# Kernel optimization log

Measured on AMD Instinct MI355X. Metric: run time of the kernel, lower is better.

The kernel has to match this reference:

```python
import jax, jax.numpy as jnp
import numpy as np

N = 16384      # batch size
F = 1024       # n_features
H = 256        # n_dim (latent)


def setup_inputs() -> dict:
    key = jax.random.key(0)
    ks = jax.random.split(key, 6)
    X = jax.random.normal(ks[0], (N, F), dtype=jnp.float32)
    We = jax.random.normal(ks[1], (F, H), dtype=jnp.float32) / np.sqrt(F).astype(np.float32)
    be = jnp.zeros((H,), dtype=jnp.float32)
    Wd = jax.random.normal(ks[2], (H, F), dtype=jnp.float32) / np.sqrt(H).astype(np.float32)
    bd = jnp.zeros((F,), dtype=jnp.float32)
    Wc = jax.random.normal(ks[3], (H, 1), dtype=jnp.float32) / np.sqrt(H).astype(np.float32)
    bc = jnp.zeros((1,), dtype=jnp.float32)
    s = jax.random.randint(ks[4], (N,), 0, 2, dtype=jnp.int32)  # protected attribute labels in {0,1}
    return {"X": X, "We": We, "be": be, "Wd": Wd, "bd": bd, "Wc": Wc, "bc": bc, "s": s, "p": 1}


def reference(X, We, be, Wd, bd, Wc, bc, s, p):
    # encoder / decoder (single Linear each, as in the default NRL construction)
    g = X @ We + be                      # [N, H]
    rec = g @ Wd + bd                    # [N, F]
    mse_mean = jnp.mean((rec - X) ** 2)  # MSELoss is built with reduction='sum' but forward uses torch.mean(pow(...)) directly

    # critic scores for ALL rows (critics share weights: [module]*n_protected)
    c = (g @ Wc + bc)[:, 0]              # [N]

    # masked pairwise L1: sum_{i in P, j notin P} |c_i - c_j|
    mp = (s == p)                        # rows where s == p
    mpf = mp.astype(c.dtype)
    mrf = (~mp).astype(c.dtype)
    Dmat = jnp.abs(c[:, None] - c[None, :])   # [N, N] pairwise L1 (cdist equivalent)
    total = mpf @ (Dmat @ mrf)                # mp^T D mr == cdist(c_p, c_rest, p=1).sum()

    w_dist_count = mp.sum()                   # == w_dist.shape[0] (number of protected rows)
    w_dist_mean = total / w_dist_count.astype(c.dtype)

    return (mse_mean, jnp.asarray(rec.shape[0]), w_dist_mean, w_dist_count)
```

## Files before the change

### kernel.cpp

```cpp
#include <hip/hip_runtime.h>
#include <hip/hip_bf16.h>
#include <cstdint>

#define NR 16384
#define NF 1024
#define NH 256

typedef __bf16 bf16x8 __attribute__((ext_vector_type(8)));
typedef float f32x4 __attribute__((ext_vector_type(4)));
typedef unsigned short us8 __attribute__((ext_vector_type(8)));

static __device__ __forceinline__ unsigned short f2bf(float f) {
    unsigned u = __float_as_uint(f);
    u += 0x7FFFu + ((u >> 16) & 1u);
    return (unsigned short)(u >> 16);
}


__global__ __launch_bounds__(256) void prep_kernel(
    const float* __restrict__ We, const float* __restrict__ Wd,
    unsigned short* __restrict__ Wepk, unsigned short* __restrict__ Wdpk,
    float* __restrict__ hdr) {
    const int b = blockIdx.x, t = threadIdx.x;
    if (b == 0 && t < 192) hdr[t] = 0.f;
    const int lane = t & 63, q = lane >> 4, li = lane & 15, idx = t >> 6;
    if (b < 16) {
        const int nb = b;
#pragma unroll
        for (int p = 0; p < 8; p++) {
            const int kc = idx + 4 * p;
            us8 v;
#pragma unroll
            for (int e = 0; e < 8; e++)
                v[e] = f2bf(We[(size_t)(kc * 32 + q * 8 + e) * NH + nb * 16 + li]);
            *(us8*)&Wepk[((size_t)(nb * 32 + kc)) * 512 + lane * 8] = v;
        }
    } else {
        const int nb4 = b - 16;
#pragma unroll
        for (int p = 0; p < 8; p++) {
            const int c = nb4 * 32 + idx + 4 * p;
            const int nb = c >> 3, kc = c & 7;
            us8 v;
#pragma unroll
            for (int e = 0; e < 8; e++)
                v[e] = f2bf(Wd[(size_t)(kc * 32 + q * 8 + e) * NF + nb * 16 + li]);
            *(us8*)&Wdpk[((size_t)(nb * 8 + kc)) * 512 + lane * 8] = v;
        }
    }
}

__global__ __launch_bounds__(256, 4) void fused_kernel(
    const float* __restrict__ X,
    const unsigned short* __restrict__ Wepk, const unsigned short* __restrict__ Wdpk,
    const float* __restrict__ be, const float* __restrict__ bd,
    const float* __restrict__ Wc, const int* __restrict__ s, const int* __restrict__ pv,
    float* __restrict__ cP, float* __restrict__ cR, float* __restrict__ hdr) {
    __shared__ union {
        unsigned short xa[32 * 512];
        struct {
            unsigned short gs[32 * 256];
            float credu[4][32];
            float msred[4];
        } p2;
    } u;
    const int t = threadIdx.x;
    const int b = blockIdx.x, m0 = b * 32;
    const int w = t >> 6, lane = t & 63, q = lane >> 4, li = lane & 15;
    const int wn = w * 64;

    const int sr = t >> 3, scg = t & 7;

    {
        const float* xrow = X + (size_t)(m0 + sr) * NF + scg * 64;
#pragma unroll
        for (int ci = 0; ci < 8; ++ci) {
            float4 lo = *(const float4*)(xrow + ci * 8);
            float4 hi = *(const float4*)(xrow + ci * 8 + 4);
            us8 v;
            v[0] = f2bf(lo.x); v[1] = f2bf(lo.y); v[2] = f2bf(lo.z); v[3] = f2bf(lo.w);
            v[4] = f2bf(hi.x); v[5] = f2bf(hi.y); v[6] = f2bf(hi.z); v[7] = f2bf(hi.w);
            const int chl = scg * 8 + ci;
            *(us8*)&u.xa[sr * 512 + ((chl ^ sr) & 63) * 8] = v;
        }
    }
    __syncthreads();

    const unsigned short* Bp[4];
#pragma unroll
    for (int j = 0; j < 4; j++)
        Bp[j] = Wepk + ((size_t)(w * 4 + j) * 32) * 512 + lane * 8;

    us8 fb[2][4];
#pragma unroll
    for (int z = 0; z < 2; ++z)
#pragma unroll
        for (int j = 0; j < 4; j++) fb[z][j] = *(const us8*)(Bp[j] + z * 512);

    f32x4 acc[2][4] = {};

#pragma unroll
    for (int k2 = 0; k2 < 16; ++k2) {
        const int kc = k2;
        const int cb = kc & 1;
        const int chl = k2 * 4 + q;
        const int ph0 = (chl ^ li) & 63;
        const int ph1 = (chl ^ (16 + li)) & 63;
        bf16x8 a0 = __builtin_bit_cast(bf16x8, *(const us8*)&u.xa[li * 512 + ph0 * 8]);
        bf16x8 a1 = __builtin_bit_cast(bf16x8, *(const us8*)&u.xa[(16 + li) * 512 + ph1 * 8]);
#pragma unroll
        for (int j = 0; j < 4; j++) {
            bf16x8 bf = __builtin_bit_cast(bf16x8, fb[cb][j]);
            acc[0][j] = __builtin_amdgcn_mfma_f32_16x16x32_bf16(bf, a0, acc[0][j], 0, 0, 0);
            acc[1][j] = __builtin_amdgcn_mfma_f32_16x16x32_bf16(bf, a1, acc[1][j], 0, 0, 0);
        }
#pragma unroll
        for (int j = 0; j < 4; j++) fb[cb][j] = *(const us8*)(Bp[j] + (kc + 2) * 512);
    }
    __syncthreads();

    {
        const float* xrow = X + (size_t)(m0 + sr) * NF + 512 + scg * 64;
#pragma unroll
        for (int ci = 0; ci < 8; ++ci) {
            float4 lo = *(const float4*)(xrow + ci * 8);
            float4 hi = *(const float4*)(xrow + ci * 8 + 4);
            us8 v;
            v[0] = f2bf(lo.x); v[1] = f2bf(lo.y); v[2] = f2bf(lo.z); v[3] = f2bf(lo.w);
            v[4] = f2bf(hi.x); v[5] = f2bf(hi.y); v[6] = f2bf(hi.z); v[7] = f2bf(hi.w);
            const int chl = scg * 8 + ci;
            *(us8*)&u.xa[sr * 512 + ((chl ^ sr) & 63) * 8] = v;
        }
    }
    __syncthreads();

#pragma unroll
    for (int k2 = 0; k2 < 16; ++k2) {
        const int kc = 16 + k2;
        const int cb = kc & 1;
        const int chl = k2 * 4 + q;
        const int ph0 = (chl ^ li) & 63;
        const int ph1 = (chl ^ (16 + li)) & 63;
        bf16x8 a0 = __builtin_bit_cast(bf16x8, *(const us8*)&u.xa[li * 512 + ph0 * 8]);
        bf16x8 a1 = __builtin_bit_cast(bf16x8, *(const us8*)&u.xa[(16 + li) * 512 + ph1 * 8]);
#pragma unroll
        for (int j = 0; j < 4; j++) {
            bf16x8 bf = __builtin_bit_cast(bf16x8, fb[cb][j]);
            acc[0][j] = __builtin_amdgcn_mfma_f32_16x16x32_bf16(bf, a0, acc[0][j], 0, 0, 0);
            acc[1][j] = __builtin_amdgcn_mfma_f32_16x16x32_bf16(bf, a1, acc[1][j], 0, 0, 0);
        }
        if (kc + 2 < 32) {
#pragma unroll
            for (int j = 0; j < 4; j++) fb[cb][j] = *(const us8*)(Bp[j] + (kc + 2) * 512);
        }
    }
    __syncthreads();

    const unsigned short* Wp = Wdpk + lane * 8;
    us8 gb[2][4];
#pragma unroll
    for (int z = 0; z < 2; ++z)
#pragma unroll
        for (int j = 0; j < 4; j++)
            gb[z][j] = *(const us8*)(Wp + ((size_t)((w * 4 + j) * 8 + z)) * 512);

#pragma unroll
    for (int i = 0; i < 2; i++) {
        float csum = 0.f;
        const int ml = i * 16 + li;
#pragma unroll
        for (int j = 0; j < 4; j++) {
            const int colb = wn + j * 16 + q * 4;
            float4 be4 = *(const float4*)&be[colb];
            float4 wc4 = *(const float4*)&Wc[colb];
            float v0 = acc[i][j][0] + be4.x;
            float v1 = acc[i][j][1] + be4.y;
            float v2 = acc[i][j][2] + be4.z;
            float v3 = acc[i][j][3] + be4.w;
            csum += v0 * wc4.x + v1 * wc4.y + v2 * wc4.z + v3 * wc4.w;
            ushort4 st = { f2bf(v0), f2bf(v1), f2bf(v2), f2bf(v3) };
            const int phys = (colb >> 3) ^ ml;
            *(ushort4*)&u.p2.gs[ml * 256 + phys * 8 + (q & 1) * 4] = st;
        }
        csum += __shfl_down(csum, 32);
        csum += __shfl_down(csum, 16);
        if (lane < 16) u.p2.credu[w][i * 16 + lane] = csum;
    }
    __syncthreads();

    if (t < 32) {
        float cs = u.p2.credu[0][t] + u.p2.credu[1][t] +
                   u.p2.credu[2][t] + u.p2.credu[3][t];
        bool pr = (s[m0 + t] == pv[0]);
        unsigned long long mk = __ballot(pr);
        int np = __popcll(mk);
        int baseP = 0, baseR = 0;
        if (t == 0) {
            baseP = atomicAdd((int*)hdr + 129, np);
            baseR = atomicAdd((int*)hdr + 130, 32 - np);
        }
        baseP = __shfl(baseP, 0);
        baseR = __shfl(baseR, 0);
        int offP = __popcll(mk & ((1ull << t) - 1ull));
        int offR = t - offP;
        if (pr) cP[baseP + offP] = cs; else cR[baseR + offR] = cs;
    }

    float lsum = 0.f;
    f32x4 a2[2][4] = {};
#pragma unroll
    for (int it = 0; it < 32; ++it) {
        const int cb = it & 1, pass = it >> 3, kc = it & 7;
        bf16x8 af[2];
#pragma unroll
        for (int i = 0; i < 2; i++) {
            const int ml = i * 16 + li;
            const int phys = (kc * 4 + q) ^ ml;
            af[i] = __builtin_bit_cast(bf16x8, *(const us8*)&u.p2.gs[ml * 256 + phys * 8]);
        }
#pragma unroll
        for (int j = 0; j < 4; j++) {
            bf16x8 bf = __builtin_bit_cast(bf16x8, gb[cb][j]);
            a2[0][j] = __builtin_amdgcn_mfma_f32_16x16x32_bf16(bf, af[0], a2[0][j], 0, 0, 0);
            a2[1][j] = __builtin_amdgcn_mfma_f32_16x16x32_bf16(bf, af[1], a2[1][j], 0, 0, 0);
        }
        if (it + 2 < 32) {
            const int p2i = (it + 2) >> 3, k2 = (it + 2) & 7;
#pragma unroll
            for (int j = 0; j < 4; j++)
                gb[cb][j] = *(const us8*)(Wp + ((size_t)((p2i * 16 + w * 4 + j) * 8 + k2)) * 512);
        }
        if (kc == 7) {
#pragma unroll
            for (int i = 0; i < 2; i++) {
                const size_t rowoff = (size_t)(m0 + i * 16 + li) * NF;
#pragma unroll
                for (int j = 0; j < 4; j++) {
                    const int colb = pass * 256 + wn + j * 16 + q * 4;
                    float4 bd4 = *(const float4*)&bd[colb];
                    float4 xr  = *(const float4*)&X[rowoff + colb];
                    float d0 = a2[i][j][0] + bd4.x - xr.x;
                    float d1 = a2[i][j][1] + bd4.y - xr.y;
                    float d2 = a2[i][j][2] + bd4.z - xr.z;
                    float d3 = a2[i][j][3] + bd4.w - xr.w;
                    lsum += d0 * d0 + d1 * d1 + d2 * d2 + d3 * d3;
                    a2[i][j] = (f32x4){0.f, 0.f, 0.f, 0.f};
                }
            }
        }
    }
#pragma unroll
    for (int o = 32; o; o >>= 1) lsum += __shfl_down(lsum, o);
    if (lane == 0) u.p2.msred[w] = lsum;
    __syncthreads();
    if (t == 0)
        atomicAdd(&hdr[b & 63], u.p2.msred[0] + u.p2.msred[1] +
                                u.p2.msred[2] + u.p2.msred[3]);
}

__global__ __launch_bounds__(256) void pair_fin_kernel(
    const float* __restrict__ cP, const float* __restrict__ cR,
    float* __restrict__ hdr, float* __restrict__ out) {
    __shared__ float sj[1024];
    __shared__ float red[256];
    __shared__ int win;
    const int nP = ((const int*)hdr)[129];
    const int nR = ((const int*)hdr)[130];
    const int jb = blockIdx.x * 1024;
    int jn = nR - jb; if (jn < 0) jn = 0; if (jn > 1024) jn = 1024;
    float sum = 0.f;
    if (jn > 0 && blockIdx.y * 512 < nP) {
        for (int j = threadIdx.x; j < 1024; j += 256)
            sj[j] = (jb + j < nR) ? cR[jb + j] : 0.f;
        __syncthreads();
        const int a0 = blockIdx.y * 512 + threadIdx.x, a1 = a0 + 256;
        const float ca0 = (a0 < nP) ? cP[a0] : 0.f;
        const float ca1 = (a1 < nP) ? cP[a1] : 0.f;
        float s0 = 0.f, s1 = 0.f;
#pragma unroll 8
        for (int j4 = 0; j4 < 256; j4++) {
            float4 v = *(const float4*)&sj[j4 * 4];
            s0 += fabsf(ca0 - v.x) + fabsf(ca0 - v.y) + fabsf(ca0 - v.z) + fabsf(ca0 - v.w);
            s1 += fabsf(ca1 - v.x) + fabsf(ca1 - v.y) + fabsf(ca1 - v.z) + fabsf(ca1 - v.w);
        }
        float pad = (float)(1024 - jn);
        s0 -= pad * fabsf(ca0);
        s1 -= pad * fabsf(ca1);
        if (a0 >= nP) s0 = 0.f;
        if (a1 >= nP) s1 = 0.f;
        sum = s0 + s1;
#pragma unroll
        for (int o = 32; o; o >>= 1) sum += __shfl_down(sum, o);
        if ((threadIdx.x & 63) == 0 && sum != 0.f)
            atomicAdd(&hdr[64 + ((blockIdx.y * 16 + blockIdx.x) & 63)], sum);
    }
    __threadfence();
    __syncthreads();
    if (threadIdx.x == 0)
        win = (atomicAdd((int*)(hdr + 128), 1) == 16 * 32 - 1) ? 1 : 0;
    __syncthreads();
    if (win) {
        float v = (threadIdx.x < 128) ? atomicAdd(&hdr[threadIdx.x], 0.f) : 0.f;
        red[threadIdx.x] = v;
        __syncthreads();
        if (threadIdx.x == 0) {
            float ms = 0.f, ps = 0.f;
            for (int i = 0; i < 64; i++) { ms += red[i]; ps += red[64 + i]; }
            int np = atomicAdd((int*)(hdr + 129), 0);
            out[0] = ms / (float)((size_t)NR * NF);
            out[1] = (float)NR;
            out[2] = ps / (float)np;
            out[3] = (float)np;
        }
    }
}

extern "C" void kernel_launch(void* const* d_in, const int* in_sizes, int n_in,
                              void* d_out, int out_size, void* d_ws, size_t ws_size,
                              hipStream_t stream) {
    const float* X  = (const float*)d_in[0];
    const float* We = (const float*)d_in[1];
    const float* be = (const float*)d_in[2];
    const float* Wd = (const float*)d_in[3];
    const float* bd = (const float*)d_in[4];
    const float* Wc = (const float*)d_in[5];
    const int*   s  = (const int*)d_in[7];
    const int*   pv = (const int*)d_in[8];

    char* ws = (char*)d_ws;
    float* hdr = (float*)ws;
    float* cP  = (float*)(ws + 1024);
    float* cR  = (float*)(ws + 1024 + 65536);
    unsigned short* Wepk = (unsigned short*)(ws + 1024 + 2 * 65536);
    unsigned short* Wdpk = Wepk + (size_t)NH * NF;

    prep_kernel<<<32, 256, 0, stream>>>(We, Wd, Wepk, Wdpk, hdr);
    fused_kernel<<<512, 256, 0, stream>>>(X, Wepk, Wdpk, be, bd, Wc, s, pv, cP, cR, hdr);
    pair_fin_kernel<<<dim3(16, 32), 256, 0, stream>>>(cP, cR, hdr, (float*)d_out);
}
```

Measured before the change: 218.7 us.

## Shrink fused kernel row tile to 16 and load full X row once

The fused encoder/decoder kernel now processes 16 rows per block instead of 32, launching 1024 blocks. The whole 1024-wide bf16 X row tile is staged into LDS in one pass rather than two halves, which removes one barrier and the mid-loop reload. This halves per-block register use for accumulators and raises block count for better occupancy and tail balance. The cost is that each weight fragment loaded from global or L2 is reused across only 16 rows, so weight traffic doubles.

```diff
diff --git a/kernel.cpp b/kernel.cpp
--- a/kernel.cpp
+++ b/kernel.cpp
@@ -50,29 +50,28 @@
     }
 }
 
-__global__ __launch_bounds__(256, 4) void fused_kernel(
+__global__ __launch_bounds__(256) void fused_kernel(
     const float* __restrict__ X,
     const unsigned short* __restrict__ Wepk, const unsigned short* __restrict__ Wdpk,
     const float* __restrict__ be, const float* __restrict__ bd,
     const float* __restrict__ Wc, const int* __restrict__ s, const int* __restrict__ pv,
     float* __restrict__ cP, float* __restrict__ cR, float* __restrict__ hdr) {
     __shared__ union {
-        unsigned short xa[32 * 512];
+        unsigned short xa[16 * 1024];
         struct {
-            unsigned short gs[32 * 256];
-            float credu[4][32];
+            unsigned short gs[16 * 256];
+            float credu[4][16];
             float msred[4];
         } p2;
     } u;
     const int t = threadIdx.x;
-    const int b = blockIdx.x, m0 = b * 32;
+    const int b = blockIdx.x, m0 = b * 16;
     const int w = t >> 6, lane = t & 63, q = lane >> 4, li = lane & 15;
     const int wn = w * 64;
 
-    const int sr = t >> 3, scg = t & 7;
-
     {
-        const float* xrow = X + (size_t)(m0 + sr) * NF + scg * 64;
+        const int r = t >> 4, cg = t & 15;
+        const float* xrow = X + (size_t)(m0 + r) * NF + cg * 64;
 #pragma unroll
         for (int ci = 0; ci < 8; ++ci) {
             float4 lo = *(const float4*)(xrow + ci * 8);
@@ -80,8 +79,8 @@
             us8 v;
             v[0] = f2bf(lo.x); v[1] = f2bf(lo.y); v[2] = f2bf(lo.z); v[3] = f2bf(lo.w);
             v[4] = f2bf(hi.x); v[5] = f2bf(hi.y); v[6] = f2bf(hi.z); v[7] = f2bf(hi.w);
-            const int chl = scg * 8 + ci;
-            *(us8*)&u.xa[sr * 512 + ((chl ^ sr) & 63) * 8] = v;
+            const int chl = cg * 8 + ci;
+            *(us8*)&u.xa[r * 1024 + ((chl ^ r) & 127) * 8] = v;
         }
     }
     __syncthreads();
@@ -97,57 +96,17 @@
 #pragma unroll
         for (int j = 0; j < 4; j++) fb[z][j] = *(const us8*)(Bp[j] + z * 512);
 
-    f32x4 acc[2][4] = {};
-
-#pragma unroll
-    for (int k2 = 0; k2 < 16; ++k2) {
-        const int kc = k2;
+    f32x4 acc[4] = {};
+#pragma unroll
+    for (int kc = 0; kc < 32; ++kc) {
         const int cb = kc & 1;
-        const int chl = k2 * 4 + q;
-        const int ph0 = (chl ^ li) & 63;
-        const int ph1 = (chl ^ (16 + li)) & 63;
-        bf16x8 a0 = __builtin_bit_cast(bf16x8, *(const us8*)&u.xa[li * 512 + ph0 * 8]);
-        bf16x8 a1 = __builtin_bit_cast(bf16x8, *(const us8*)&u.xa[(16 + li) * 512 + ph1 * 8]);
+        const int chl = kc * 4 + q;
+        const int ph0 = (chl ^ li) & 127;
+        bf16x8 a0 = __builtin_bit_cast(bf16x8, *(const us8*)&u.xa[li * 1024 + ph0 * 8]);
 #pragma unroll
         for (int j = 0; j < 4; j++) {
             bf16x8 bf = __builtin_bit_cast(bf16x8, fb[cb][j]);
-            acc[0][j] = __builtin_amdgcn_mfma_f32_16x16x32_bf16(bf, a0, acc[0][j], 0, 0, 0);
-            acc[1][j] = __builtin_amdgcn_mfma_f32_16x16x32_bf16(bf, a1, acc[1][j], 0, 0, 0);
-        }
-#pragma unroll
-        for (int j = 0; j < 4; j++) fb[cb][j] = *(const us8*)(Bp[j] + (kc + 2) * 512);
-    }
-    __syncthreads();
-
-    {
-        const float* xrow = X + (size_t)(m0 + sr) * NF + 512 + scg * 64;
-#pragma unroll
-        for (int ci = 0; ci < 8; ++ci) {
-            float4 lo = *(const float4*)(xrow + ci * 8);
-            float4 hi = *(const float4*)(xrow + ci * 8 + 4);
-            us8 v;
-            v[0] = f2bf(lo.x); v[1] = f2bf(lo.y); v[2] = f2bf(lo.z); v[3] = f2bf(lo.w);
-            v[4] = f2bf(hi.x); v[5] = f2bf(hi.y); v[6] = f2bf(hi.z); v[7] = f2bf(hi.w);
-            const int chl = scg * 8 + ci;
-            *(us8*)&u.xa[sr * 512 + ((chl ^ sr) & 63) * 8] = v;
-        }
-    }
-    __syncthreads();
-
-#pragma unroll
-    for (int k2 = 0; k2 < 16; ++k2) {
-        const int kc = 16 + k2;
-        const int cb = kc & 1;
-        const int chl = k2 * 4 + q;
-        const int ph0 = (chl ^ li) & 63;
-        const int ph1 = (chl ^ (16 + li)) & 63;
-        bf16x8 a0 = __builtin_bit_cast(bf16x8, *(const us8*)&u.xa[li * 512 + ph0 * 8]);
-        bf16x8 a1 = __builtin_bit_cast(bf16x8, *(const us8*)&u.xa[(16 + li) * 512 + ph1 * 8]);
-#pragma unroll
-        for (int j = 0; j < 4; j++) {
-            bf16x8 bf = __builtin_bit_cast(bf16x8, fb[cb][j]);
-            acc[0][j] = __builtin_amdgcn_mfma_f32_16x16x32_bf16(bf, a0, acc[0][j], 0, 0, 0);
-            acc[1][j] = __builtin_amdgcn_mfma_f32_16x16x32_bf16(bf, a1, acc[1][j], 0, 0, 0);
+            acc[j] = __builtin_amdgcn_mfma_f32_16x16x32_bf16(bf, a0, acc[j], 0, 0, 0);
         }
         if (kc + 2 < 32) {
 #pragma unroll
@@ -164,19 +123,18 @@
         for (int j = 0; j < 4; j++)
             gb[z][j] = *(const us8*)(Wp + ((size_t)((w * 4 + j) * 8 + z)) * 512);
 
-#pragma unroll
-    for (int i = 0; i < 2; i++) {
+    {
         float csum = 0.f;
-        const int ml = i * 16 + li;
+        const int ml = li;
 #pragma unroll
         for (int j = 0; j < 4; j++) {
             const int colb = wn + j * 16 + q * 4;
             float4 be4 = *(const float4*)&be[colb];
             float4 wc4 = *(const float4*)&Wc[colb];
-            float v0 = acc[i][j][0] + be4.x;
-            float v1 = acc[i][j][1] + be4.y;
-            float v2 = acc[i][j][2] + be4.z;
-            float v3 = acc[i][j][3] + be4.w;
+            float v0 = acc[j][0] + be4.x;
+            float v1 = acc[j][1] + be4.y;
+            float v2 = acc[j][2] + be4.z;
+            float v3 = acc[j][3] + be4.w;
             csum += v0 * wc4.x + v1 * wc4.y + v2 * wc4.z + v3 * wc4.w;
             ushort4 st = { f2bf(v0), f2bf(v1), f2bf(v2), f2bf(v3) };
             const int phys = (colb >> 3) ^ ml;
@@ -184,11 +142,11 @@
         }
         csum += __shfl_down(csum, 32);
         csum += __shfl_down(csum, 16);
-        if (lane < 16) u.p2.credu[w][i * 16 + lane] = csum;
-    }
-    __syncthreads();
-
-    if (t < 32) {
+        if (lane < 16) u.p2.credu[w][lane] = csum;
+    }
+    __syncthreads();
+
+    if (t < 16) {
         float cs = u.p2.credu[0][t] + u.p2.credu[1][t] +
                    u.p2.credu[2][t] + u.p2.credu[3][t];
         bool pr = (s[m0 + t] == pv[0]);
@@ -197,7 +155,7 @@
         int baseP = 0, baseR = 0;
         if (t == 0) {
             baseP = atomicAdd((int*)hdr + 129, np);
-            baseR = atomicAdd((int*)hdr + 130, 32 - np);
+            baseR = atomicAdd((int*)hdr + 130, 16 - np);
         }
         baseP = __shfl(baseP, 0);
         baseR = __shfl(baseR, 0);
@@ -207,22 +165,17 @@
     }
 
     float lsum = 0.f;
-    f32x4 a2[2][4] = {};
+    f32x4 a2[4] = {};
 #pragma unroll
     for (int it = 0; it < 32; ++it) {
         const int cb = it & 1, pass = it >> 3, kc = it & 7;
-        bf16x8 af[2];
-#pragma unroll
-        for (int i = 0; i < 2; i++) {
-            const int ml = i * 16 + li;
-            const int phys = (kc * 4 + q) ^ ml;
-            af[i] = __builtin_bit_cast(bf16x8, *(const us8*)&u.p2.gs[ml * 256 + phys * 8]);
-        }
+        const int ml = li;
+        const int phys = (kc * 4 + q) ^ ml;
+        bf16x8 af = __builtin_bit_cast(bf16x8, *(const us8*)&u.p2.gs[ml * 256 + phys * 8]);
 #pragma unroll
         for (int j = 0; j < 4; j++) {
             bf16x8 bf = __builtin_bit_cast(bf16x8, gb[cb][j]);
-            a2[0][j] = __builtin_amdgcn_mfma_f32_16x16x32_bf16(bf, af[0], a2[0][j], 0, 0, 0);
-            a2[1][j] = __builtin_amdgcn_mfma_f32_16x16x32_bf16(bf, af[1], a2[1][j], 0, 0, 0);
+            a2[j] = __builtin_amdgcn_mfma_f32_16x16x32_bf16(bf, af, a2[j], 0, 0, 0);
         }
         if (it + 2 < 32) {
             const int p2i = (it + 2) >> 3, k2 = (it + 2) & 7;
@@ -231,21 +184,18 @@
                 gb[cb][j] = *(const us8*)(Wp + ((size_t)((p2i * 16 + w * 4 + j) * 8 + k2)) * 512);
         }
         if (kc == 7) {
-#pragma unroll
-            for (int i = 0; i < 2; i++) {
-                const size_t rowoff = (size_t)(m0 + i * 16 + li) * NF;
-#pragma unroll
-                for (int j = 0; j < 4; j++) {
-                    const int colb = pass * 256 + wn + j * 16 + q * 4;
-                    float4 bd4 = *(const float4*)&bd[colb];
-                    float4 xr  = *(const float4*)&X[rowoff + colb];
-                    float d0 = a2[i][j][0] + bd4.x - xr.x;
-                    float d1 = a2[i][j][1] + bd4.y - xr.y;
-                    float d2 = a2[i][j][2] + bd4.z - xr.z;
-                    float d3 = a2[i][j][3] + bd4.w - xr.w;
-                    lsum += d0 * d0 + d1 * d1 + d2 * d2 + d3 * d3;
-                    a2[i][j] = (f32x4){0.f, 0.f, 0.f, 0.f};
-                }
+            const size_t rowoff = (size_t)(m0 + li) * NF;
+#pragma unroll
+            for (int j = 0; j < 4; j++) {
+                const int colb = pass * 256 + wn + j * 16 + q * 4;
+                float4 bd4 = *(const float4*)&bd[colb];
+                float4 xr  = *(const float4*)&X[rowoff + colb];
+                float d0 = a2[j][0] + bd4.x - xr.x;
+                float d1 = a2[j][1] + bd4.y - xr.y;
+                float d2 = a2[j][2] + bd4.z - xr.z;
+                float d3 = a2[j][3] + bd4.w - xr.w;
+                lsum += d0 * d0 + d1 * d1 + d2 * d2 + d3 * d3;
+                a2[j] = (f32x4){0.f, 0.f, 0.f, 0.f};
             }
         }
     }
@@ -335,6 +285,6 @@
     unsigned short* Wdpk = Wepk + (size_t)NH * NF;
 
     prep_kernel<<<32, 256, 0, stream>>>(We, Wd, Wepk, Wdpk, hdr);
-    fused_kernel<<<512, 256, 0, stream>>>(X, Wepk, Wdpk, be, bd, Wc, s, pv, cP, cR, hdr);
+    fused_kernel<<<1024, 256, 0, stream>>>(X, Wepk, Wdpk, be, bd, Wc, s, pv, cP, cR, hdr);
     pair_fin_kernel<<<dim3(16, 32), 256, 0, stream>>>(cP, cR, hdr, (float*)d_out);
 }
```

Measured after the change: 214.4 us. Within noise of the previous version (-1.9%).
